# Kernel optimization log

Measured on AMD Instinct MI355X. Metric: run time of the kernel, lower is better.

## Reference

```python
import jax, jax.numpy as jnp
import numpy as np

TNEI = 2
TOPK = 4
NEIGH = 2 * TNEI + 1  # window size = 5


def _normalize(x, eps=1e-12):
    # matches torch F.normalize(dim=-1)
    n = jnp.linalg.norm(x, axis=-1, keepdims=True)
    return x / jnp.maximum(n, eps)


def setup_inputs() -> dict:
    key = jax.random.key(0)
    ks = jax.random.split(key, 10)
    B, T, C = 32, 256, 128
    x = jax.random.normal(ks[0], (B, T, C), jnp.float32)
    radj = jax.random.randint(ks[1], (B, T, T), 0, 2).astype(jnp.int32)
    inxs = jax.random.randint(ks[2], (B, T, TOPK), 0, T)
    s = 1.0 / np.sqrt(C)
    W_pf = jax.random.normal(ks[3], (C, C), jnp.float32) * s
    W_ns = jax.random.normal(ks[4], (C, C), jnp.float32) * s
    W_v = jax.random.normal(ks[5], (C, C), jnp.float32) * s
    v_pf = jax.random.normal(ks[6], (NEIGH,), jnp.float32)
    g_pf = jnp.linalg.norm(v_pf)[None]  # weight_norm gain, shape (1,)
    v_ns = jax.random.normal(ks[7], (TOPK,), jnp.float32)
    g_ns = jnp.linalg.norm(v_ns)[None]
    return dict(x=x, radj=radj, inxs=inxs, W_pf=W_pf, W_ns=W_ns, W_v=W_v,
                v_pf=v_pf, g_pf=g_pf, v_ns=v_ns, g_ns=g_ns)


def reference(x, radj, inxs, W_pf, W_ns, W_v, v_pf, g_pf, v_ns, g_ns):
    B, T, C = x.shape
    pf = _normalize(x @ W_pf.T)
    ns = _normalize(x @ W_ns.T)
    v = x @ W_v.T
    # windowed neighbor indices, identical to _tneigh_mask(mode='all')
    i = jnp.arange(T)
    start = jnp.clip(i - TNEI, 0, T - NEIGH)
    nbr = start[:, None] + jnp.arange(NEIGH)[None, :]  # (T, NEIGH)
    ctx = pf[:, nbr]  # (B, T, NEIGH, C) — replaces one-hot ctxinx einsum
    # pairwise window similarity: (B,T,T,n,n)
    sim = jnp.einsum('bxic,byjc->bxyij', ctx, ctx)
    # AdaptiveMaxPool2d((n,1)) == max over the last (key-window) axis
    sim_pf = sim.max(axis=-1)  # (B,T,T,n)
    w_pf = g_pf[0] * v_pf / jnp.linalg.norm(v_pf)  # weight-norm agg_pf
    sim_pf = jnp.einsum('bxyi,i->bxy', sim_pf, w_pf)
    # topk-neighbor branch: inxs gathers ns rows (replaces one-hot einsum)
    ns_q = ns[jnp.arange(B)[:, None, None], inxs]  # (B,T,TOPK,C)
    sim_ns = jnp.einsum('bxnc,byc->bxyn', ns_q, ns)  # (B,T,T,TOPK)
    w_ns = g_ns[0] * v_ns / jnp.linalg.norm(v_ns)  # weight-norm agg_ns
    sim_ns = jnp.einsum('bxyn,n->bxy', sim_ns, w_ns)
    # adjacency mask: 0 -> -1e22, >0 -> 0
    mask = jnp.where(radj == 0, jnp.float32(-1e22), jnp.float32(0.0))
    attn = jax.nn.softmax(sim_pf + sim_ns + mask, axis=-1)  # (B,T,T)
    return jnp.einsum('bkt,btd->bkd', attn, v)  # (B,T,C)
```

## Files before the change

kernel.cpp:

```cpp
#include <hip/hip_runtime.h>
#include <math.h>


#define TT 256
#define CC 128

using bf16x8 = __attribute__((ext_vector_type(8))) short;
using f32x4  = __attribute__((ext_vector_type(4))) float;

__device__ __forceinline__ short bf_hi(float x) {
    unsigned u = __float_as_uint(x);
    return (short)((u + 0x7FFFu + ((u >> 16) & 1u)) >> 16);
}
__device__ __forceinline__ void bf_split(float x, short& h, short& l) {
    h = bf_hi(x);
    float hf = __uint_as_float(((unsigned)(unsigned short)h) << 16);
    l = bf_hi(x - hf);
}
__device__ __forceinline__ float max5(float a, float b, float c, float d, float e) {
    return fmaxf(fmaxf(fmaxf(a, b), fmaxf(c, d)), e);
}

__global__ __launch_bounds__(256, 4) void proj_kernel(
    const float* __restrict__ x,
    const float* __restrict__ W0, const float* __restrict__ W1, const float* __restrict__ W2,
    float* __restrict__ pf, float* __restrict__ ns,
    short* __restrict__ vt_h, short* __restrict__ vt_l)
{
    __shared__ short Ah[32 * 40], Al[32 * 40];
    __shared__ short Bh[128 * 40], Bl[128 * 40];
    __shared__ float ssb[32][4];
    const int tid = threadIdx.x;
    const int row0 = blockIdx.x * 32;
    const int m = blockIdx.y;
    const float* __restrict__ W = (m == 0) ? W0 : (m == 1) ? W1 : W2;
    const int lane = tid & 63, wn = tid >> 6;
    const int quad = lane >> 4, lr = lane & 15;
    f32x4 z4 = {0.f, 0.f, 0.f, 0.f};
    f32x4 acc[2][2] = {{z4, z4}, {z4, z4}};

    for (int k0 = 0; k0 < CC; k0 += 32) {
        __syncthreads();
        {
            int r = tid >> 3, q = (tid & 7) * 4;
            float4 a4 = *(const float4*)&x[(row0 + r) * CC + k0 + q];
            short4 h4, l4;
            bf_split(a4.x, h4.x, l4.x); bf_split(a4.y, h4.y, l4.y);
            bf_split(a4.z, h4.z, l4.z); bf_split(a4.w, h4.w, l4.w);
            *(short4*)&Ah[r * 40 + q] = h4; *(short4*)&Al[r * 40 + q] = l4;
        }
        for (int i = 0; i < 4; i++) {
            int flat = i * 256 + tid, r = flat >> 3, q = (flat & 7) * 4;
            float4 b4 = *(const float4*)&W[r * CC + k0 + q];
            short4 h4, l4;
            bf_split(b4.x, h4.x, l4.x); bf_split(b4.y, h4.y, l4.y);
            bf_split(b4.z, h4.z, l4.z); bf_split(b4.w, h4.w, l4.w);
            *(short4*)&Bh[r * 40 + q] = h4; *(short4*)&Bl[r * 40 + q] = l4;
        }
        __syncthreads();
        bf16x8 ah[2], al[2], bh[2], bl[2];
        for (int ra = 0; ra < 2; ra++) {
            int ar = (16 * ra + lr) * 40 + quad * 8;
            ah[ra] = *(bf16x8*)&Ah[ar];
            al[ra] = *(bf16x8*)&Al[ar];
        }
        for (int tn = 0; tn < 2; tn++) {
            int br = (32 * wn + 16 * tn + lr) * 40 + quad * 8;
            bh[tn] = *(bf16x8*)&Bh[br];
            bl[tn] = *(bf16x8*)&Bl[br];
        }
        for (int ra = 0; ra < 2; ra++)
            for (int tn = 0; tn < 2; tn++) {
                acc[ra][tn] = __builtin_amdgcn_mfma_f32_16x16x32_bf16(ah[ra], bh[tn], acc[ra][tn], 0, 0, 0);
                acc[ra][tn] = __builtin_amdgcn_mfma_f32_16x16x32_bf16(ah[ra], bl[tn], acc[ra][tn], 0, 0, 0);
                acc[ra][tn] = __builtin_amdgcn_mfma_f32_16x16x32_bf16(al[ra], bh[tn], acc[ra][tn], 0, 0, 0);
            }
    }
    if (m < 2) {
        float* __restrict__ o = (m == 0) ? pf : ns;
        float ssp[2][4];
        for (int ra = 0; ra < 2; ra++)
            for (int reg = 0; reg < 4; reg++) {
                float s = acc[ra][0][reg] * acc[ra][0][reg]
                        + acc[ra][1][reg] * acc[ra][1][reg];
                for (int off = 1; off < 16; off <<= 1) s += __shfl_xor(s, off);
                ssp[ra][reg] = s;
            }
        if (lr == 0)
            for (int ra = 0; ra < 2; ra++)
                for (int reg = 0; reg < 4; reg++)
                    ssb[16 * ra + quad * 4 + reg][wn] = ssp[ra][reg];
        __syncthreads();
        for (int ra = 0; ra < 2; ra++)
            for (int reg = 0; reg < 4; reg++) {
                int ml = 16 * ra + quad * 4 + reg;
                float ss = ssb[ml][0] + ssb[ml][1] + ssb[ml][2] + ssb[ml][3];
                float inv = 1.f / fmaxf(sqrtf(ss), 1e-12f);
                int row = row0 + ml;
                for (int tn = 0; tn < 2; tn++)
                    o[row * CC + 32 * wn + 16 * tn + lr] = acc[ra][tn][reg] * inv;
            }
    } else {
        for (int ra = 0; ra < 2; ra++) {
            int rowbase = row0 + 16 * ra + quad * 4;
            int b = rowbase >> 8, t0 = rowbase & 255;
            for (int tn = 0; tn < 2; tn++) {
                int c = 32 * wn + 16 * tn + lr;
                short4 h4, l4;
                for (int reg = 0; reg < 4; reg++)
                    bf_split(acc[ra][tn][reg], ((short*)&h4)[reg], ((short*)&l4)[reg]);
                size_t o = ((size_t)b * CC + c) * TT + t0;
                *(short4*)&vt_h[o] = h4;
                *(short4*)&vt_l[o] = l4;
            }
        }
    }
}

__global__ __launch_bounds__(256, 4) void gram_mfma(
    const float* __restrict__ pf, const float* __restrict__ ns,
    const int* __restrict__ inxs, const float* __restrict__ v_ns,
    const float* __restrict__ g_ns, float* __restrict__ G, float* __restrict__ S)
{
    __shared__ short Ah[64 * 40], Al[64 * 40], Bh[64 * 40], Bl[64 * 40];
    const int tid = threadIdx.x;
    const int m0 = blockIdx.x * 64, n0 = blockIdx.y * 64;
    const int b = blockIdx.z >> 1, half = blockIdx.z & 1;
    const float* __restrict__ Pb = pf + (size_t)b * TT * CC;
    const float* __restrict__ Nb = ns + (size_t)b * TT * CC;
    const float* __restrict__ Bsrc = half ? Nb : Pb;

    float w0 = 0.f, w1 = 0.f, w2 = 0.f, w3 = 0.f;
    int4 id0 = {0, 0, 0, 0}, id1 = {0, 0, 0, 0};
    if (half) {
        float n2 = v_ns[0]*v_ns[0] + v_ns[1]*v_ns[1] + v_ns[2]*v_ns[2] + v_ns[3]*v_ns[3];
        float sc = g_ns[0] / sqrtf(n2);
        w0 = sc*v_ns[0]; w1 = sc*v_ns[1]; w2 = sc*v_ns[2]; w3 = sc*v_ns[3];
        id0 = *(const int4*)&inxs[(b * TT + m0 + (tid >> 3)) * 4];
        id1 = *(const int4*)&inxs[(b * TT + m0 + 32 + (tid >> 3)) * 4];
    }

    const int lane = tid & 63, wave = tid >> 6;
    const int wm = wave >> 1, wn = wave & 1;
    const int quad = lane >> 4, lr = lane & 15;
    f32x4 z4 = {0.f, 0.f, 0.f, 0.f};
    f32x4 acc[2][2] = {{z4, z4}, {z4, z4}};

    for (int k0 = 0; k0 < CC; k0 += 32) {
        __syncthreads();
        for (int i = 0; i < 2; i++) {
            int flat = i * 256 + tid, r = flat >> 3, q = (flat & 7) * 4;
            float4 a4;
            if (!half) {
                a4 = *(const float4*)&Pb[(m0 + r) * CC + k0 + q];
            } else {
                int4 id = i ? id1 : id0;
                float4 aa = *(const float4*)&Nb[id.x * CC + k0 + q];
                float4 ab = *(const float4*)&Nb[id.y * CC + k0 + q];
                float4 ac = *(const float4*)&Nb[id.z * CC + k0 + q];
                float4 ad = *(const float4*)&Nb[id.w * CC + k0 + q];
                a4.x = w0*aa.x + w1*ab.x + w2*ac.x + w3*ad.x;
                a4.y = w0*aa.y + w1*ab.y + w2*ac.y + w3*ad.y;
                a4.z = w0*aa.z + w1*ab.z + w2*ac.z + w3*ad.z;
                a4.w = w0*aa.w + w1*ab.w + w2*ac.w + w3*ad.w;
            }
            float4 b4 = *(const float4*)&Bsrc[(n0 + r) * CC + k0 + q];
            short4 h4, l4;
            bf_split(a4.x, h4.x, l4.x); bf_split(a4.y, h4.y, l4.y);
            bf_split(a4.z, h4.z, l4.z); bf_split(a4.w, h4.w, l4.w);
            *(short4*)&Ah[r * 40 + q] = h4; *(short4*)&Al[r * 40 + q] = l4;
            bf_split(b4.x, h4.x, l4.x); bf_split(b4.y, h4.y, l4.y);
            bf_split(b4.z, h4.z, l4.z); bf_split(b4.w, h4.w, l4.w);
            *(short4*)&Bh[r * 40 + q] = h4; *(short4*)&Bl[r * 40 + q] = l4;
        }
        __syncthreads();
        bf16x8 bh[2], bl[2];
        for (int tn = 0; tn < 2; tn++) {
            int br = (32 * wn + 16 * tn + lr) * 40 + quad * 8;
            bh[tn] = *(bf16x8*)&Bh[br];
            bl[tn] = *(bf16x8*)&Bl[br];
        }
        for (int tm = 0; tm < 2; tm++) {
            int ar = (32 * wm + 16 * tm + lr) * 40 + quad * 8;
            bf16x8 ah = *(bf16x8*)&Ah[ar];
            bf16x8 al = *(bf16x8*)&Al[ar];
            for (int tn = 0; tn < 2; tn++) {
                acc[tm][tn] = __builtin_amdgcn_mfma_f32_16x16x32_bf16(ah, bh[tn], acc[tm][tn], 0, 0, 0);
                acc[tm][tn] = __builtin_amdgcn_mfma_f32_16x16x32_bf16(ah, bl[tn], acc[tm][tn], 0, 0, 0);
                acc[tm][tn] = __builtin_amdgcn_mfma_f32_16x16x32_bf16(al, bh[tn], acc[tm][tn], 0, 0, 0);
            }
        }
    }
    float* __restrict__ Cb = (half ? S : G) + (size_t)b * TT * TT;
    for (int tm = 0; tm < 2; tm++)
        for (int tn = 0; tn < 2; tn++) {
            int rb = m0 + 32 * wm + 16 * tm + quad * 4;
            int cb = n0 + 32 * wn + 16 * tn + lr;
            for (int reg = 0; reg < 4; reg++)
                Cb[(size_t)(rb + reg) * TT + cb] = acc[tm][tn][reg];
        }
}

__global__ __launch_bounds__(256, 2) void fused_smax_pv(
    const float* __restrict__ G, const float* __restrict__ S,
    const int* __restrict__ radj, const float* __restrict__ v_pf,
    const float* __restrict__ g_pf,
    const short* __restrict__ vt_h, const short* __restrict__ vt_l,
    float* __restrict__ out)
{
    __shared__ float Gs[20 * 256];
    __shared__ float RM[20 * 256];
    __shared__ short ATH[16 * 264];
    __shared__ short ATL[16 * 264];
    __shared__ float RD[64];
    __shared__ float RMX[64];
    const int tid = threadIdx.x;
    const int xt = blockIdx.x, b = blockIdx.y;
    const int x0 = xt * 16;
    const int rbase = min(max(x0 - 2, 0), TT - 5);
    for (int i = 0; i < 5; i++) {
        int flat = i * 256 + tid, ri = flat >> 6, q = (flat & 63) * 4;
        int r = min(rbase + ri, TT - 1);
        *(float4*)&Gs[ri * 256 + q] = *(const float4*)&G[(size_t)b * TT * TT + r * TT + q];
    }
    float n2 = 0.f;
    for (int i = 0; i < 5; i++) n2 += v_pf[i] * v_pf[i];
    float sc = g_pf[0] / sqrtf(n2);
    float wpf[5];
    for (int i = 0; i < 5; i++) wpf[i] = sc * v_pf[i];
    __syncthreads();
    for (int t = 0; t < 5; t++) {
        int task = t * 256 + tid;
        int i = task >> 6, g = task & 63;
        const float* row = &Gs[i * 256];
        float4 X = *(float4*)&row[4 * g];
        float m0_, m1_, m2_, m3_;
        if (g == 0) {
            float4 N = *(float4*)&row[4];
            float mx = fmaxf(fmaxf(X.x, X.y), fmaxf(X.z, X.w));
            m0_ = m1_ = m2_ = fmaxf(mx, N.x);
            m3_ = max5(X.y, X.z, X.w, N.x, N.y);
        } else if (g == 63) {
            float4 P = *(float4*)&row[248];
            m0_ = max5(P.z, P.w, X.x, X.y, X.z);
            float mx = fmaxf(fmaxf(X.x, X.y), fmaxf(X.z, X.w));
            m1_ = m2_ = m3_ = fmaxf(P.w, mx);
        } else {
            float4 P = *(float4*)&row[4 * g - 4];
            float4 N = *(float4*)&row[4 * g + 4];
            m0_ = max5(P.z, P.w, X.x, X.y, X.z);
            m1_ = max5(P.w, X.x, X.y, X.z, X.w);
            m2_ = max5(X.x, X.y, X.z, X.w, N.x);
            m3_ = max5(X.y, X.z, X.w, N.x, N.y);
        }
        float4 o4 = {m0_, m1_, m2_, m3_};
        *(float4*)&RM[i * 256 + 4 * g] = o4;
    }
    __syncthreads();
    const int y = tid;
    const size_t sb = (size_t)b * TT * TT;
    float lv[16];
    if (xt > 0 && xt < 15) {
        float rm[20];
        #pragma unroll
        for (int r = 0; r < 20; r++) rm[r] = RM[r * 256 + y];
        #pragma unroll
        for (int xi = 0; xi < 16; xi++) {
            float s = wpf[0] * rm[xi];
            #pragma unroll
            for (int i = 1; i < 5; i++) s = fmaf(wpf[i], rm[xi + i], s);
            lv[xi] = s;
        }
    } else {
        for (int xi = 0; xi < 16; xi++) {
            int sxr = min(max(x0 + xi - 2, 0), TT - 5) - rbase;
            float s = 0.f;
            for (int i = 0; i < 5; i++) s = fmaf(wpf[i], RM[(sxr + i) * 256 + y], s);
            lv[xi] = s;
        }
    }
    for (int xi = 0; xi < 16; xi++) {
        lv[xi] += S[sb + (x0 + xi) * TT + y];
        if (radj[sb + (x0 + xi) * TT + y] == 0) lv[xi] += -1e22f;
    }
    const int lane = tid & 63, wv = tid >> 6;
    for (int xi = 0; xi < 16; xi++) {
        float v = lv[xi];
        for (int o = 32; o; o >>= 1) v = fmaxf(v, __shfl_xor(v, o));
        if (lane == 0) RMX[xi * 4 + wv] = v;
    }
    __syncthreads();
    for (int xi = 0; xi < 16; xi++) {
        float mx = fmaxf(fmaxf(RMX[xi * 4], RMX[xi * 4 + 1]),
                         fmaxf(RMX[xi * 4 + 2], RMX[xi * 4 + 3]));
        float e = __expf(lv[xi] - mx);
        short h, l;
        bf_split(e, h, l);
        ATH[xi * 264 + y] = h;
        ATL[xi * 264 + y] = l;
        for (int o = 32; o; o >>= 1) e += __shfl_xor(e, o);
        if (lane == 0) RD[xi * 4 + wv] = e;
    }
    __syncthreads();
    const int quad = lane >> 4, lr = lane & 15;
    const int c0 = wv * 32;
    const short* __restrict__ vhb = vt_h + (size_t)b * CC * TT;
    const short* __restrict__ vlb = vt_l + (size_t)b * CC * TT;
    const int ar0 = (c0 + lr) * TT, ar1 = ar0 + 16 * TT;
    f32x4 z4 = {0.f, 0.f, 0.f, 0.f};
    f32x4 acc[2] = {z4, z4};
    #pragma unroll
    for (int k0 = 0; k0 < TT; k0 += 32) {
        int ko = k0 + quad * 8;
        bf16x8 bh = *(bf16x8*)&ATH[lr * 264 + ko];
        bf16x8 bl = *(bf16x8*)&ATL[lr * 264 + ko];
        bf16x8 a0h = *(const bf16x8*)&vhb[ar0 + ko];
        bf16x8 a0l = *(const bf16x8*)&vlb[ar0 + ko];
        bf16x8 a1h = *(const bf16x8*)&vhb[ar1 + ko];
        bf16x8 a1l = *(const bf16x8*)&vlb[ar1 + ko];
        acc[0] = __builtin_amdgcn_mfma_f32_16x16x32_bf16(a0h, bh, acc[0], 0, 0, 0);
        acc[0] = __builtin_amdgcn_mfma_f32_16x16x32_bf16(a0h, bl, acc[0], 0, 0, 0);
        acc[0] = __builtin_amdgcn_mfma_f32_16x16x32_bf16(a0l, bh, acc[0], 0, 0, 0);
        acc[1] = __builtin_amdgcn_mfma_f32_16x16x32_bf16(a1h, bh, acc[1], 0, 0, 0);
        acc[1] = __builtin_amdgcn_mfma_f32_16x16x32_bf16(a1h, bl, acc[1], 0, 0, 0);
        acc[1] = __builtin_amdgcn_mfma_f32_16x16x32_bf16(a1l, bh, acc[1], 0, 0, 0);
    }
    float sm = RD[lr * 4] + RD[lr * 4 + 1] + RD[lr * 4 + 2] + RD[lr * 4 + 3];
    float rinv = 1.f / sm;
    for (int tm = 0; tm < 2; tm++) {
        float4 r;
        r.x = acc[tm][0] * rinv; r.y = acc[tm][1] * rinv;
        r.z = acc[tm][2] * rinv; r.w = acc[tm][3] * rinv;
        *(float4*)&out[(size_t)b * TT * CC + (x0 + lr) * CC + c0 + 16 * tm + quad * 4] = r;
    }
}

extern "C" void kernel_launch(void* const* d_in, const int* in_sizes, int n_in,
                              void* d_out, int out_size, void* d_ws, size_t ws_size,
                              hipStream_t stream) {
    const float* x    = (const float*)d_in[0];
    const int*   radj = (const int*)d_in[1];
    const int*   inxs = (const int*)d_in[2];
    const float* Wpf  = (const float*)d_in[3];
    const float* Wns  = (const float*)d_in[4];
    const float* Wv   = (const float*)d_in[5];
    const float* v_pf = (const float*)d_in[6];
    const float* g_pf = (const float*)d_in[7];
    const float* v_ns = (const float*)d_in[8];
    const float* g_ns = (const float*)d_in[9];
    float* out = (float*)d_out;

    char* base = (char*)d_ws;
    float* pf   = (float*)(base);
    float* ns   = (float*)(base + (4u << 20));
    short* vt_h = (short*)(base + (8u << 20));
    short* vt_l = (short*)(base + (10u << 20));
    float* G    = (float*)(base + (12u << 20));
    float* S    = (float*)(base + (20u << 20));

    proj_kernel<<<dim3(256, 3), 256, 0, stream>>>(x, Wpf, Wns, Wv, pf, ns, vt_h, vt_l);
    gram_mfma<<<dim3(4, 4, 64), 256, 0, stream>>>(pf, ns, inxs, v_ns, g_ns, G, S);
    fused_smax_pv<<<dim3(16, 32), 256, 0, stream>>>(G, S, radj, v_pf, g_pf,
                                                    vt_h, vt_l, out);
}
```

Measured before the change: 124.8 us.

## Pre-split operands to bf16 hi/lo and load MFMA fragments straight from global

Adds a small kernel that splits the weights into bf16 hi/lo once, and makes the projection kernel write pf and ns already split into hi/lo. The projection and gram kernels then load MFMA fragments directly from global memory instead of staging through LDS with __syncthreads, keeping LDS staging only for the gathered ns_q side. The softmax kernel now reads G rows directly rather than copying them to shared memory, and issues the S and radj loads early. This trades LDS staging and barriers for uncached, less coalesced global fragment loads, and adds one extra kernel launch.

```diff
diff --git a/kernel.cpp b/kernel.cpp
--- a/kernel.cpp
+++ b/kernel.cpp
@@ -17,57 +17,66 @@
     float hf = __uint_as_float(((unsigned)(unsigned short)h) << 16);
     l = bf_hi(x - hf);
 }
+__device__ __forceinline__ void split8(const float* __restrict__ p, bf16x8& h, bf16x8& l) {
+    float4 a = *(const float4*)p;
+    float4 b = *(const float4*)(p + 4);
+    short sh, sl;
+    bf_split(a.x, sh, sl); h[0] = sh; l[0] = sl;
+    bf_split(a.y, sh, sl); h[1] = sh; l[1] = sl;
+    bf_split(a.z, sh, sl); h[2] = sh; l[2] = sl;
+    bf_split(a.w, sh, sl); h[3] = sh; l[3] = sl;
+    bf_split(b.x, sh, sl); h[4] = sh; l[4] = sl;
+    bf_split(b.y, sh, sl); h[5] = sh; l[5] = sl;
+    bf_split(b.z, sh, sl); h[6] = sh; l[6] = sl;
+    bf_split(b.w, sh, sl); h[7] = sh; l[7] = sl;
+}
 __device__ __forceinline__ float max5(float a, float b, float c, float d, float e) {
     return fmaxf(fmaxf(fmaxf(a, b), fmaxf(c, d)), e);
 }
 
-__global__ __launch_bounds__(256, 4) void proj_kernel(
+__global__ __launch_bounds__(256) void wsplit_kernel(
+    const float* __restrict__ W0, const float* __restrict__ W1, const float* __restrict__ W2,
+    short* __restrict__ Wh, short* __restrict__ Wl)
+{
+    const int m = blockIdx.y;
+    const float* __restrict__ W = (m == 0) ? W0 : (m == 1) ? W1 : W2;
+    int i = (blockIdx.x * 256 + threadIdx.x) * 4;
+    float4 a = *(const float4*)&W[i];
+    short4 h, l;
+    bf_split(a.x, h.x, l.x); bf_split(a.y, h.y, l.y);
+    bf_split(a.z, h.z, l.z); bf_split(a.w, h.w, l.w);
+    *(short4*)&Wh[m * CC * CC + i] = h;
+    *(short4*)&Wl[m * CC * CC + i] = l;
+}
+
+__global__ __launch_bounds__(256, 3) void proj_kernel(
     const float* __restrict__ x,
-    const float* __restrict__ W0, const float* __restrict__ W1, const float* __restrict__ W2,
-    float* __restrict__ pf, float* __restrict__ ns,
+    const short* __restrict__ Wh, const short* __restrict__ Wl,
+    short* __restrict__ pfh, short* __restrict__ pfl,
+    float* __restrict__ nsf, short* __restrict__ nsh, short* __restrict__ nsl,
     short* __restrict__ vt_h, short* __restrict__ vt_l)
 {
-    __shared__ short Ah[32 * 40], Al[32 * 40];
-    __shared__ short Bh[128 * 40], Bl[128 * 40];
     __shared__ float ssb[32][4];
     const int tid = threadIdx.x;
     const int row0 = blockIdx.x * 32;
     const int m = blockIdx.y;
-    const float* __restrict__ W = (m == 0) ? W0 : (m == 1) ? W1 : W2;
+    const short* __restrict__ Whm = Wh + m * CC * CC;
+    const short* __restrict__ Wlm = Wl + m * CC * CC;
     const int lane = tid & 63, wn = tid >> 6;
     const int quad = lane >> 4, lr = lane & 15;
     f32x4 z4 = {0.f, 0.f, 0.f, 0.f};
     f32x4 acc[2][2] = {{z4, z4}, {z4, z4}};
 
+    #pragma unroll 2
     for (int k0 = 0; k0 < CC; k0 += 32) {
-        __syncthreads();
-        {
-            int r = tid >> 3, q = (tid & 7) * 4;
-            float4 a4 = *(const float4*)&x[(row0 + r) * CC + k0 + q];
-            short4 h4, l4;
-            bf_split(a4.x, h4.x, l4.x); bf_split(a4.y, h4.y, l4.y);
-            bf_split(a4.z, h4.z, l4.z); bf_split(a4.w, h4.w, l4.w);
-            *(short4*)&Ah[r * 40 + q] = h4; *(short4*)&Al[r * 40 + q] = l4;
-        }
-        for (int i = 0; i < 4; i++) {
-            int flat = i * 256 + tid, r = flat >> 3, q = (flat & 7) * 4;
-            float4 b4 = *(const float4*)&W[r * CC + k0 + q];
-            short4 h4, l4;
-            bf_split(b4.x, h4.x, l4.x); bf_split(b4.y, h4.y, l4.y);
-            bf_split(b4.z, h4.z, l4.z); bf_split(b4.w, h4.w, l4.w);
-            *(short4*)&Bh[r * 40 + q] = h4; *(short4*)&Bl[r * 40 + q] = l4;
-        }
-        __syncthreads();
+        const int ko = k0 + quad * 8;
         bf16x8 ah[2], al[2], bh[2], bl[2];
-        for (int ra = 0; ra < 2; ra++) {
-            int ar = (16 * ra + lr) * 40 + quad * 8;
-            ah[ra] = *(bf16x8*)&Ah[ar];
-            al[ra] = *(bf16x8*)&Al[ar];
-        }
+        for (int ra = 0; ra < 2; ra++)
+            split8(&x[(size_t)(row0 + 16 * ra + lr) * CC + ko], ah[ra], al[ra]);
         for (int tn = 0; tn < 2; tn++) {
-            int br = (32 * wn + 16 * tn + lr) * 40 + quad * 8;
-            bh[tn] = *(bf16x8*)&Bh[br];
-            bl[tn] = *(bf16x8*)&Bl[br];
+            int br = (32 * wn + 16 * tn + lr) * CC + ko;
+            bh[tn] = *(const bf16x8*)&Whm[br];
+            bl[tn] = *(const bf16x8*)&Wlm[br];
         }
         for (int ra = 0; ra < 2; ra++)
             for (int tn = 0; tn < 2; tn++) {
@@ -77,7 +86,6 @@
             }
     }
     if (m < 2) {
-        float* __restrict__ o = (m == 0) ? pf : ns;
         float ssp[2][4];
         for (int ra = 0; ra < 2; ra++)
             for (int reg = 0; reg < 4; reg++) {
@@ -97,8 +105,15 @@
                 float ss = ssb[ml][0] + ssb[ml][1] + ssb[ml][2] + ssb[ml][3];
                 float inv = 1.f / fmaxf(sqrtf(ss), 1e-12f);
                 int row = row0 + ml;
-                for (int tn = 0; tn < 2; tn++)
-                    o[row * CC + 32 * wn + 16 * tn + lr] = acc[ra][tn][reg] * inv;
+                for (int tn = 0; tn < 2; tn++) {
+                    int col = 32 * wn + 16 * tn + lr;
+                    float val = acc[ra][tn][reg] * inv;
+                    short h, l;
+                    bf_split(val, h, l);
+                    size_t o = (size_t)row * CC + col;
+                    if (m == 0) { pfh[o] = h; pfl[o] = l; }
+                    else        { nsf[o] = val; nsh[o] = h; nsl[o] = l; }
+                }
             }
     } else {
         for (int ra = 0; ra < 2; ra++) {
@@ -118,76 +133,93 @@
 }
 
 __global__ __launch_bounds__(256, 4) void gram_mfma(
-    const float* __restrict__ pf, const float* __restrict__ ns,
+    const short* __restrict__ pfh, const short* __restrict__ pfl,
+    const float* __restrict__ nsf,
+    const short* __restrict__ nsh, const short* __restrict__ nsl,
     const int* __restrict__ inxs, const float* __restrict__ v_ns,
     const float* __restrict__ g_ns, float* __restrict__ G, float* __restrict__ S)
 {
-    __shared__ short Ah[64 * 40], Al[64 * 40], Bh[64 * 40], Bl[64 * 40];
+    __shared__ short Ah[64 * 40], Al[64 * 40];
     const int tid = threadIdx.x;
     const int m0 = blockIdx.x * 64, n0 = blockIdx.y * 64;
     const int b = blockIdx.z >> 1, half = blockIdx.z & 1;
-    const float* __restrict__ Pb = pf + (size_t)b * TT * CC;
-    const float* __restrict__ Nb = ns + (size_t)b * TT * CC;
-    const float* __restrict__ Bsrc = half ? Nb : Pb;
-
-    float w0 = 0.f, w1 = 0.f, w2 = 0.f, w3 = 0.f;
-    int4 id0 = {0, 0, 0, 0}, id1 = {0, 0, 0, 0};
-    if (half) {
-        float n2 = v_ns[0]*v_ns[0] + v_ns[1]*v_ns[1] + v_ns[2]*v_ns[2] + v_ns[3]*v_ns[3];
-        float sc = g_ns[0] / sqrtf(n2);
-        w0 = sc*v_ns[0]; w1 = sc*v_ns[1]; w2 = sc*v_ns[2]; w3 = sc*v_ns[3];
-        id0 = *(const int4*)&inxs[(b * TT + m0 + (tid >> 3)) * 4];
-        id1 = *(const int4*)&inxs[(b * TT + m0 + 32 + (tid >> 3)) * 4];
-    }
-
+    const size_t base = (size_t)b * TT * CC;
+    const short* __restrict__ Bhg = (half ? nsh : pfh) + base;
+    const short* __restrict__ Blg = (half ? nsl : pfl) + base;
     const int lane = tid & 63, wave = tid >> 6;
     const int wm = wave >> 1, wn = wave & 1;
     const int quad = lane >> 4, lr = lane & 15;
     f32x4 z4 = {0.f, 0.f, 0.f, 0.f};
     f32x4 acc[2][2] = {{z4, z4}, {z4, z4}};
-
-    for (int k0 = 0; k0 < CC; k0 += 32) {
-        __syncthreads();
-        for (int i = 0; i < 2; i++) {
-            int flat = i * 256 + tid, r = flat >> 3, q = (flat & 7) * 4;
-            float4 a4;
-            if (!half) {
-                a4 = *(const float4*)&Pb[(m0 + r) * CC + k0 + q];
-            } else {
+    const int brow0 = (n0 + 32 * wn + lr) * CC;
+
+    if (!half) {
+        const short* __restrict__ Ahg = pfh + base;
+        const short* __restrict__ Alg = pfl + base;
+        const int arow0 = (m0 + 32 * wm + lr) * CC;
+        #pragma unroll 2
+        for (int k0 = 0; k0 < CC; k0 += 32) {
+            const int ko = k0 + quad * 8;
+            bf16x8 ah[2], al[2], bh[2], bl[2];
+            for (int tm = 0; tm < 2; tm++) {
+                ah[tm] = *(const bf16x8*)&Ahg[arow0 + tm * 16 * CC + ko];
+                al[tm] = *(const bf16x8*)&Alg[arow0 + tm * 16 * CC + ko];
+            }
+            for (int tn = 0; tn < 2; tn++) {
+                bh[tn] = *(const bf16x8*)&Bhg[brow0 + tn * 16 * CC + ko];
+                bl[tn] = *(const bf16x8*)&Blg[brow0 + tn * 16 * CC + ko];
+            }
+            for (int tm = 0; tm < 2; tm++)
+                for (int tn = 0; tn < 2; tn++) {
+                    acc[tm][tn] = __builtin_amdgcn_mfma_f32_16x16x32_bf16(ah[tm], bh[tn], acc[tm][tn], 0, 0, 0);
+                    acc[tm][tn] = __builtin_amdgcn_mfma_f32_16x16x32_bf16(ah[tm], bl[tn], acc[tm][tn], 0, 0, 0);
+                    acc[tm][tn] = __builtin_amdgcn_mfma_f32_16x16x32_bf16(al[tm], bh[tn], acc[tm][tn], 0, 0, 0);
+                }
+        }
+    } else {
+        float n2 = v_ns[0]*v_ns[0] + v_ns[1]*v_ns[1] + v_ns[2]*v_ns[2] + v_ns[3]*v_ns[3];
+        float sc = g_ns[0] / sqrtf(n2);
+        float w0 = sc*v_ns[0], w1 = sc*v_ns[1], w2 = sc*v_ns[2], w3 = sc*v_ns[3];
+        int4 id0 = *(const int4*)&inxs[(b * TT + m0 + (tid >> 3)) * 4];
+        int4 id1 = *(const int4*)&inxs[(b * TT + m0 + 32 + (tid >> 3)) * 4];
+        const float* __restrict__ Nf = nsf + base;
+
+        for (int k0 = 0; k0 < CC; k0 += 32) {
+            __syncthreads();
+            for (int i = 0; i < 2; i++) {
+                int flat = i * 256 + tid, r = flat >> 3, q = (flat & 7) * 4;
                 int4 id = i ? id1 : id0;
-                float4 aa = *(const float4*)&Nb[id.x * CC + k0 + q];
-                float4 ab = *(const float4*)&Nb[id.y * CC + k0 + q];
-                float4 ac = *(const float4*)&Nb[id.z * CC + k0 + q];
-                float4 ad = *(const float4*)&Nb[id.w * CC + k0 + q];
+                float4 aa = *(const float4*)&Nf[id.x * CC + k0 + q];
+                float4 ab = *(const float4*)&Nf[id.y * CC + k0 + q];
+                float4 ac = *(const float4*)&Nf[id.z * CC + k0 + q];
+                float4 ad = *(const float4*)&Nf[id.w * CC + k0 + q];
+                float4 a4;
                 a4.x = w0*aa.x + w1*ab.x + w2*ac.x + w3*ad.x;
                 a4.y = w0*aa.y + w1*ab.y + w2*ac.y + w3*ad.y;
                 a4.z = w0*aa.z + w1*ab.z + w2*ac.z + w3*ad.z;
                 a4.w = w0*aa.w + w1*ab.w + w2*ac.w + w3*ad.w;
-            }
-            float4 b4 = *(const float4*)&Bsrc[(n0 + r) * CC + k0 + q];
-            short4 h4, l4;
-            bf_split(a4.x, h4.x, l4.x); bf_split(a4.y, h4.y, l4.y);
-            bf_split(a4.z, h4.z, l4.z); bf_split(a4.w, h4.w, l4.w);
-            *(short4*)&Ah[r * 40 + q] = h4; *(short4*)&Al[r * 40 + q] = l4;
-            bf_split(b4.x, h4.x, l4.x); bf_split(b4.y, h4.y, l4.y);
-            bf_split(b4.z, h4.z, l4.z); bf_split(b4.w, h4.w, l4.w);
-            *(short4*)&Bh[r * 40 + q] = h4; *(short4*)&Bl[r * 40 + q] = l4;
-        }
-        __syncthreads();
-        bf16x8 bh[2], bl[2];
-        for (int tn = 0; tn < 2; tn++) {
-            int br = (32 * wn + 16 * tn + lr) * 40 + quad * 8;
-            bh[tn] = *(bf16x8*)&Bh[br];
-            bl[tn] = *(bf16x8*)&Bl[br];
-        }
-        for (int tm = 0; tm < 2; tm++) {
-            int ar = (32 * wm + 16 * tm + lr) * 40 + quad * 8;
-            bf16x8 ah = *(bf16x8*)&Ah[ar];
-            bf16x8 al = *(bf16x8*)&Al[ar];
+                short4 h4, l4;
+                bf_split(a4.x, h4.x, l4.x); bf_split(a4.y, h4.y, l4.y);
+                bf_split(a4.z, h4.z, l4.z); bf_split(a4.w, h4.w, l4.w);
+                *(short4*)&Ah[r * 40 + q] = h4;
+                *(short4*)&Al[r * 40 + q] = l4;
+            }
+            __syncthreads();
+            const int ko = k0 + quad * 8;
+            bf16x8 bh[2], bl[2];
             for (int tn = 0; tn < 2; tn++) {
-                acc[tm][tn] = __builtin_amdgcn_mfma_f32_16x16x32_bf16(ah, bh[tn], acc[tm][tn], 0, 0, 0);
-                acc[tm][tn] = __builtin_amdgcn_mfma_f32_16x16x32_bf16(ah, bl[tn], acc[tm][tn], 0, 0, 0);
-                acc[tm][tn] = __builtin_amdgcn_mfma_f32_16x16x32_bf16(al, bh[tn], acc[tm][tn], 0, 0, 0);
+                bh[tn] = *(const bf16x8*)&Bhg[brow0 + tn * 16 * CC + ko];
+                bl[tn] = *(const bf16x8*)&Blg[brow0 + tn * 16 * CC + ko];
+            }
+            for (int tm = 0; tm < 2; tm++) {
+                int ar = (32 * wm + 16 * tm + lr) * 40 + quad * 8;
+                bf16x8 ah = *(bf16x8*)&Ah[ar];
+                bf16x8 al = *(bf16x8*)&Al[ar];
+                for (int tn = 0; tn < 2; tn++) {
+                    acc[tm][tn] = __builtin_amdgcn_mfma_f32_16x16x32_bf16(ah, bh[tn], acc[tm][tn], 0, 0, 0);
+                    acc[tm][tn] = __builtin_amdgcn_mfma_f32_16x16x32_bf16(ah, bl[tn], acc[tm][tn], 0, 0, 0);
+                    acc[tm][tn] = __builtin_amdgcn_mfma_f32_16x16x32_bf16(al, bh[tn], acc[tm][tn], 0, 0, 0);
+                }
             }
         }
     }
@@ -208,7 +240,6 @@
     const short* __restrict__ vt_h, const short* __restrict__ vt_l,
     float* __restrict__ out)
 {
-    __shared__ float Gs[20 * 256];
     __shared__ float RM[20 * 256];
     __shared__ short ATH[16 * 264];
     __shared__ short ATL[16 * 264];
@@ -218,36 +249,41 @@
     const int xt = blockIdx.x, b = blockIdx.y;
     const int x0 = xt * 16;
     const int rbase = min(max(x0 - 2, 0), TT - 5);
-    for (int i = 0; i < 5; i++) {
-        int flat = i * 256 + tid, ri = flat >> 6, q = (flat & 63) * 4;
-        int r = min(rbase + ri, TT - 1);
-        *(float4*)&Gs[ri * 256 + q] = *(const float4*)&G[(size_t)b * TT * TT + r * TT + q];
+    const int y = tid;
+    const size_t sb = (size_t)b * TT * TT;
+
+    float sadd[16];
+    #pragma unroll
+    for (int xi = 0; xi < 16; xi++) {
+        float s = S[sb + (x0 + xi) * TT + y];
+        int a = radj[sb + (x0 + xi) * TT + y];
+        sadd[xi] = s + ((a == 0) ? -1e22f : 0.f);
     }
     float n2 = 0.f;
     for (int i = 0; i < 5; i++) n2 += v_pf[i] * v_pf[i];
     float sc = g_pf[0] / sqrtf(n2);
     float wpf[5];
     for (int i = 0; i < 5; i++) wpf[i] = sc * v_pf[i];
-    __syncthreads();
+
     for (int t = 0; t < 5; t++) {
         int task = t * 256 + tid;
         int i = task >> 6, g = task & 63;
-        const float* row = &Gs[i * 256];
-        float4 X = *(float4*)&row[4 * g];
+        const float* __restrict__ row = &G[sb + (size_t)min(rbase + i, TT - 1) * TT];
+        float4 X = *(const float4*)&row[4 * g];
         float m0_, m1_, m2_, m3_;
         if (g == 0) {
-            float4 N = *(float4*)&row[4];
+            float4 N = *(const float4*)&row[4];
             float mx = fmaxf(fmaxf(X.x, X.y), fmaxf(X.z, X.w));
             m0_ = m1_ = m2_ = fmaxf(mx, N.x);
             m3_ = max5(X.y, X.z, X.w, N.x, N.y);
         } else if (g == 63) {
-            float4 P = *(float4*)&row[248];
+            float4 P = *(const float4*)&row[248];
             m0_ = max5(P.z, P.w, X.x, X.y, X.z);
             float mx = fmaxf(fmaxf(X.x, X.y), fmaxf(X.z, X.w));
             m1_ = m2_ = m3_ = fmaxf(P.w, mx);
         } else {
-            float4 P = *(float4*)&row[4 * g - 4];
-            float4 N = *(float4*)&row[4 * g + 4];
+            float4 P = *(const float4*)&row[4 * g - 4];
+            float4 N = *(const float4*)&row[4 * g + 4];
             m0_ = max5(P.z, P.w, X.x, X.y, X.z);
             m1_ = max5(P.w, X.x, X.y, X.z, X.w);
             m2_ = max5(X.x, X.y, X.z, X.w, N.x);
@@ -257,8 +293,6 @@
         *(float4*)&RM[i * 256 + 4 * g] = o4;
     }
     __syncthreads();
-    const int y = tid;
-    const size_t sb = (size_t)b * TT * TT;
     float lv[16];
     if (xt > 0 && xt < 15) {
         float rm[20];
@@ -269,19 +303,15 @@
             float s = wpf[0] * rm[xi];
             #pragma unroll
             for (int i = 1; i < 5; i++) s = fmaf(wpf[i], rm[xi + i], s);
-            lv[xi] = s;
+            lv[xi] = s + sadd[xi];
         }
     } else {
         for (int xi = 0; xi < 16; xi++) {
             int sxr = min(max(x0 + xi - 2, 0), TT - 5) - rbase;
             float s = 0.f;
             for (int i = 0; i < 5; i++) s = fmaf(wpf[i], RM[(sxr + i) * 256 + y], s);
-            lv[xi] = s;
-        }
-    }
-    for (int xi = 0; xi < 16; xi++) {
-        lv[xi] += S[sb + (x0 + xi) * TT + y];
-        if (radj[sb + (x0 + xi) * TT + y] == 0) lv[xi] += -1e22f;
+            lv[xi] = s + sadd[xi];
+        }
     }
     const int lane = tid & 63, wv = tid >> 6;
     for (int xi = 0; xi < 16; xi++) {
@@ -351,15 +381,21 @@
     float* out = (float*)d_out;
 
     char* base = (char*)d_ws;
-    float* pf   = (float*)(base);
-    float* ns   = (float*)(base + (4u << 20));
-    short* vt_h = (short*)(base + (8u << 20));
-    short* vt_l = (short*)(base + (10u << 20));
-    float* G    = (float*)(base + (12u << 20));
-    float* S    = (float*)(base + (20u << 20));
-
-    proj_kernel<<<dim3(256, 3), 256, 0, stream>>>(x, Wpf, Wns, Wv, pf, ns, vt_h, vt_l);
-    gram_mfma<<<dim3(4, 4, 64), 256, 0, stream>>>(pf, ns, inxs, v_ns, g_ns, G, S);
+    short* pfh  = (short*)(base);
+    short* pfl  = (short*)(base + (2u << 20));
+    short* nsh  = (short*)(base + (4u << 20));
+    short* nsl  = (short*)(base + (6u << 20));
+    float* nsf  = (float*)(base + (8u << 20));
+    short* vt_h = (short*)(base + (12u << 20));
+    short* vt_l = (short*)(base + (14u << 20));
+    float* G    = (float*)(base + (16u << 20));
+    float* S    = (float*)(base + (24u << 20));
+    short* Wh   = (short*)(base + (32u << 20));
+    short* Wl   = (short*)(base + (33u << 20));
+
+    wsplit_kernel<<<dim3(16, 3), 256, 0, stream>>>(Wpf, Wns, Wv, Wh, Wl);
+    proj_kernel<<<dim3(256, 3), 256, 0, stream>>>(x, Wh, Wl, pfh, pfl, nsf, nsh, nsl, vt_h, vt_l);
+    gram_mfma<<<dim3(4, 4, 64), 256, 0, stream>>>(pfh, pfl, nsf, nsh, nsl, inxs, v_ns, g_ns, G, S);
     fused_smax_pv<<<dim3(16, 32), 256, 0, stream>>>(G, S, radj, v_pf, g_pf,
                                                     vt_h, vt_l, out);
 }
```

After: 135.4 us. 1.08x slower.

## Precompute bf16 hi/lo splits for weights and normalized pf/ns features

Applied to the files above, without the earlier changes.

Adds a small kernel that splits the three weight matrices into bf16 hi/lo once per call, so the projection kernel loads ready-made bf16 pairs instead of re-splitting W in each of its 768 blocks. The projection epilogue now writes pf and ns directly as bf16 hi/lo, keeping an fp32 copy of ns for the weighted top-k gather. The Gram kernel then copies pre-split operands into shared memory instead of converting fp32 every tile. This removes repeated split arithmetic but adds an extra launch and changes the workspace layout.

```diff
diff --git a/kernel.cpp b/kernel.cpp
--- a/kernel.cpp
+++ b/kernel.cpp
@@ -21,10 +21,26 @@
     return fmaxf(fmaxf(fmaxf(a, b), fmaxf(c, d)), e);
 }
 
+__global__ __launch_bounds__(256) void wsplit_kernel(
+    const float* __restrict__ W0, const float* __restrict__ W1, const float* __restrict__ W2,
+    short* __restrict__ Wh, short* __restrict__ Wl)
+{
+    const int m = blockIdx.y;
+    const float* __restrict__ W = (m == 0) ? W0 : (m == 1) ? W1 : W2;
+    int i = (blockIdx.x * 256 + threadIdx.x) * 4;
+    float4 a = *(const float4*)&W[i];
+    short4 h, l;
+    bf_split(a.x, h.x, l.x); bf_split(a.y, h.y, l.y);
+    bf_split(a.z, h.z, l.z); bf_split(a.w, h.w, l.w);
+    *(short4*)&Wh[m * CC * CC + i] = h;
+    *(short4*)&Wl[m * CC * CC + i] = l;
+}
+
 __global__ __launch_bounds__(256, 4) void proj_kernel(
     const float* __restrict__ x,
-    const float* __restrict__ W0, const float* __restrict__ W1, const float* __restrict__ W2,
-    float* __restrict__ pf, float* __restrict__ ns,
+    const short* __restrict__ Wh, const short* __restrict__ Wl,
+    short* __restrict__ pfh, short* __restrict__ pfl,
+    float* __restrict__ nsf, short* __restrict__ nsh, short* __restrict__ nsl,
     short* __restrict__ vt_h, short* __restrict__ vt_l)
 {
     __shared__ short Ah[32 * 40], Al[32 * 40];
@@ -33,7 +49,8 @@
     const int tid = threadIdx.x;
     const int row0 = blockIdx.x * 32;
     const int m = blockIdx.y;
-    const float* __restrict__ W = (m == 0) ? W0 : (m == 1) ? W1 : W2;
+    const short* __restrict__ Whm = Wh + m * CC * CC;
+    const short* __restrict__ Wlm = Wl + m * CC * CC;
     const int lane = tid & 63, wn = tid >> 6;
     const int quad = lane >> 4, lr = lane & 15;
     f32x4 z4 = {0.f, 0.f, 0.f, 0.f};
@@ -51,11 +68,8 @@
         }
         for (int i = 0; i < 4; i++) {
             int flat = i * 256 + tid, r = flat >> 3, q = (flat & 7) * 4;
-            float4 b4 = *(const float4*)&W[r * CC + k0 + q];
-            short4 h4, l4;
-            bf_split(b4.x, h4.x, l4.x); bf_split(b4.y, h4.y, l4.y);
-            bf_split(b4.z, h4.z, l4.z); bf_split(b4.w, h4.w, l4.w);
-            *(short4*)&Bh[r * 40 + q] = h4; *(short4*)&Bl[r * 40 + q] = l4;
+            *(short4*)&Bh[r * 40 + q] = *(const short4*)&Whm[r * CC + k0 + q];
+            *(short4*)&Bl[r * 40 + q] = *(const short4*)&Wlm[r * CC + k0 + q];
         }
         __syncthreads();
         bf16x8 ah[2], al[2], bh[2], bl[2];
@@ -77,7 +91,6 @@
             }
     }
     if (m < 2) {
-        float* __restrict__ o = (m == 0) ? pf : ns;
         float ssp[2][4];
         for (int ra = 0; ra < 2; ra++)
             for (int reg = 0; reg < 4; reg++) {
@@ -97,8 +110,15 @@
                 float ss = ssb[ml][0] + ssb[ml][1] + ssb[ml][2] + ssb[ml][3];
                 float inv = 1.f / fmaxf(sqrtf(ss), 1e-12f);
                 int row = row0 + ml;
-                for (int tn = 0; tn < 2; tn++)
-                    o[row * CC + 32 * wn + 16 * tn + lr] = acc[ra][tn][reg] * inv;
+                for (int tn = 0; tn < 2; tn++) {
+                    int col = 32 * wn + 16 * tn + lr;
+                    float val = acc[ra][tn][reg] * inv;
+                    short h, l;
+                    bf_split(val, h, l);
+                    size_t o = (size_t)row * CC + col;
+                    if (m == 0) { pfh[o] = h; pfl[o] = l; }
+                    else        { nsf[o] = val; nsh[o] = h; nsl[o] = l; }
+                }
             }
     } else {
         for (int ra = 0; ra < 2; ra++) {
@@ -118,7 +138,9 @@
 }
 
 __global__ __launch_bounds__(256, 4) void gram_mfma(
-    const float* __restrict__ pf, const float* __restrict__ ns,
+    const short* __restrict__ pfh, const short* __restrict__ pfl,
+    const float* __restrict__ nsf,
+    const short* __restrict__ nsh, const short* __restrict__ nsl,
     const int* __restrict__ inxs, const float* __restrict__ v_ns,
     const float* __restrict__ g_ns, float* __restrict__ G, float* __restrict__ S)
 {
@@ -126,9 +148,9 @@
     const int tid = threadIdx.x;
     const int m0 = blockIdx.x * 64, n0 = blockIdx.y * 64;
     const int b = blockIdx.z >> 1, half = blockIdx.z & 1;
-    const float* __restrict__ Pb = pf + (size_t)b * TT * CC;
-    const float* __restrict__ Nb = ns + (size_t)b * TT * CC;
-    const float* __restrict__ Bsrc = half ? Nb : Pb;
+    const size_t base = (size_t)b * TT * CC;
+    const short* __restrict__ Bhg = (half ? nsh : pfh) + base;
+    const short* __restrict__ Blg = (half ? nsl : pfl) + base;
 
     float w0 = 0.f, w1 = 0.f, w2 = 0.f, w3 = 0.f;
     int4 id0 = {0, 0, 0, 0}, id1 = {0, 0, 0, 0};
@@ -145,33 +167,41 @@
     const int quad = lane >> 4, lr = lane & 15;
     f32x4 z4 = {0.f, 0.f, 0.f, 0.f};
     f32x4 acc[2][2] = {{z4, z4}, {z4, z4}};
+    const short* __restrict__ Ahg = pfh + base;
+    const short* __restrict__ Alg = pfl + base;
+    const float* __restrict__ Nf = nsf + base;
 
     for (int k0 = 0; k0 < CC; k0 += 32) {
         __syncthreads();
-        for (int i = 0; i < 2; i++) {
-            int flat = i * 256 + tid, r = flat >> 3, q = (flat & 7) * 4;
-            float4 a4;
-            if (!half) {
-                a4 = *(const float4*)&Pb[(m0 + r) * CC + k0 + q];
-            } else {
+        if (!half) {
+            for (int i = 0; i < 2; i++) {
+                int flat = i * 256 + tid, r = flat >> 3, q = (flat & 7) * 4;
+                *(short4*)&Ah[r * 40 + q] = *(const short4*)&Ahg[(m0 + r) * CC + k0 + q];
+                *(short4*)&Al[r * 40 + q] = *(const short4*)&Alg[(m0 + r) * CC + k0 + q];
+                *(short4*)&Bh[r * 40 + q] = *(const short4*)&Bhg[(n0 + r) * CC + k0 + q];
+                *(short4*)&Bl[r * 40 + q] = *(const short4*)&Blg[(n0 + r) * CC + k0 + q];
+            }
+        } else {
+            for (int i = 0; i < 2; i++) {
+                int flat = i * 256 + tid, r = flat >> 3, q = (flat & 7) * 4;
                 int4 id = i ? id1 : id0;
-                float4 aa = *(const float4*)&Nb[id.x * CC + k0 + q];
-                float4 ab = *(const float4*)&Nb[id.y * CC + k0 + q];
-                float4 ac = *(const float4*)&Nb[id.z * CC + k0 + q];
-                float4 ad = *(const float4*)&Nb[id.w * CC + k0 + q];
+                float4 aa = *(const float4*)&Nf[id.x * CC + k0 + q];
+                float4 ab = *(const float4*)&Nf[id.y * CC + k0 + q];
+                float4 ac = *(const float4*)&Nf[id.z * CC + k0 + q];
+                float4 ad = *(const float4*)&Nf[id.w * CC + k0 + q];
+                float4 a4;
                 a4.x = w0*aa.x + w1*ab.x + w2*ac.x + w3*ad.x;
                 a4.y = w0*aa.y + w1*ab.y + w2*ac.y + w3*ad.y;
                 a4.z = w0*aa.z + w1*ab.z + w2*ac.z + w3*ad.z;
                 a4.w = w0*aa.w + w1*ab.w + w2*ac.w + w3*ad.w;
-            }
-            float4 b4 = *(const float4*)&Bsrc[(n0 + r) * CC + k0 + q];
-            short4 h4, l4;
-            bf_split(a4.x, h4.x, l4.x); bf_split(a4.y, h4.y, l4.y);
-            bf_split(a4.z, h4.z, l4.z); bf_split(a4.w, h4.w, l4.w);
-            *(short4*)&Ah[r * 40 + q] = h4; *(short4*)&Al[r * 40 + q] = l4;
-            bf_split(b4.x, h4.x, l4.x); bf_split(b4.y, h4.y, l4.y);
-            bf_split(b4.z, h4.z, l4.z); bf_split(b4.w, h4.w, l4.w);
-            *(short4*)&Bh[r * 40 + q] = h4; *(short4*)&Bl[r * 40 + q] = l4;
+                short4 h4, l4;
+                bf_split(a4.x, h4.x, l4.x); bf_split(a4.y, h4.y, l4.y);
+                bf_split(a4.z, h4.z, l4.z); bf_split(a4.w, h4.w, l4.w);
+                *(short4*)&Ah[r * 40 + q] = h4;
+                *(short4*)&Al[r * 40 + q] = l4;
+                *(short4*)&Bh[r * 40 + q] = *(const short4*)&Bhg[(n0 + r) * CC + k0 + q];
+                *(short4*)&Bl[r * 40 + q] = *(const short4*)&Blg[(n0 + r) * CC + k0 + q];
+            }
         }
         __syncthreads();
         bf16x8 bh[2], bl[2];
@@ -351,15 +381,21 @@
     float* out = (float*)d_out;
 
     char* base = (char*)d_ws;
-    float* pf   = (float*)(base);
-    float* ns   = (float*)(base + (4u << 20));
-    short* vt_h = (short*)(base + (8u << 20));
-    short* vt_l = (short*)(base + (10u << 20));
-    float* G    = (float*)(base + (12u << 20));
-    float* S    = (float*)(base + (20u << 20));
-
-    proj_kernel<<<dim3(256, 3), 256, 0, stream>>>(x, Wpf, Wns, Wv, pf, ns, vt_h, vt_l);
-    gram_mfma<<<dim3(4, 4, 64), 256, 0, stream>>>(pf, ns, inxs, v_ns, g_ns, G, S);
+    short* pfh  = (short*)(base);
+    short* pfl  = (short*)(base + (2u << 20));
+    short* nsh  = (short*)(base + (4u << 20));
+    short* nsl  = (short*)(base + (6u << 20));
+    float* nsf  = (float*)(base + (8u << 20));
+    short* vt_h = (short*)(base + (12u << 20));
+    short* vt_l = (short*)(base + (14u << 20));
+    float* G    = (float*)(base + (16u << 20));
+    float* S    = (float*)(base + (24u << 20));
+    short* Wh   = (short*)(base + (32u << 20));
+    short* Wl   = (short*)(base + (33u << 20));
+
+    wsplit_kernel<<<dim3(16, 3), 256, 0, stream>>>(Wpf, Wns, Wv, Wh, Wl);
+    proj_kernel<<<dim3(256, 3), 256, 0, stream>>>(x, Wh, Wl, pfh, pfl, nsf, nsh, nsl, vt_h, vt_l);
+    gram_mfma<<<dim3(4, 4, 64), 256, 0, stream>>>(pfh, pfl, nsf, nsh, nsl, inxs, v_ns, g_ns, G, S);
     fused_smax_pv<<<dim3(16, 32), 256, 0, stream>>>(G, S, radj, v_pf, g_pf,
                                                     vt_h, vt_l, out);
 }
```

Result: slower. 129.7 us (+3.9%).
